# Kernel tuning notes

Measured on AMD Instinct MI355X. Metric: run time of the kernel, lower is better.

Reference implementation:

```python
import jax, jax.numpy as jnp
import numpy as np

HIDDEN = 64
HALF = 32
VOCAB = 64
B, L = 256, 2048


def _l2norm(x):
    # matches torch F.normalize(dim=-1, eps=1e-12)
    return x / jnp.maximum(jnp.linalg.norm(x, axis=-1, keepdims=True), 1e-12)


def setup_inputs() -> dict:
    key = jax.random.key(0)
    ks = jax.random.split(key, 16)
    s = 0.02
    return {
        "seq": jax.random.randint(ks[0], (B, L), 0, VOCAB),
        "embed": jax.random.normal(ks[1], (VOCAB, HIDDEN), jnp.float32) * s,
        "W1": jax.random.normal(ks[2], (2 * HIDDEN, HIDDEN), jnp.float32) * s,
        "b1": jnp.zeros((2 * HIDDEN,), jnp.float32),
        "W2": jax.random.normal(ks[3], (HIDDEN, 2 * HIDDEN), jnp.float32) * s,
        "b2": jnp.zeros((HIDDEN,), jnp.float32),
        "ln_g": jnp.ones((HIDDEN,), jnp.float32),
        "ln_b": jnp.zeros((HIDDEN,), jnp.float32),
        "Ws": jax.random.normal(ks[4], (HALF, HIDDEN), jnp.float32) * s,
        "bs": jnp.zeros((HALF,), jnp.float32),
        "We": jax.random.normal(ks[5], (HALF, HIDDEN), jnp.float32) * s,
        "be": jnp.zeros((HALF,), jnp.float32),
        "Wrp": jax.random.normal(ks[6], (HIDDEN, 2 * HALF), jnp.float32) * s,
        "brp": jnp.zeros((HIDDEN,), jnp.float32),
        "Wo": jax.random.normal(ks[7], (VOCAB, HIDDEN), jnp.float32) * s,
        "bo": jnp.zeros((VOCAB,), jnp.float32),
    }


def reference(seq, embed, W1, b1, W2, b2, ln_g, ln_b, Ws, bs, We, be, Wrp, brp, Wo, bo):
    # Encoder: embed -> LayerNorm(h + FF(h))
    h0 = embed[seq]                                     # [B,L,H]
    ff = jnp.maximum(h0 @ W1.T + b1, 0.0) @ W2.T + b2
    x = h0 + ff
    mu = x.mean(-1, keepdims=True)
    var = x.var(-1, keepdims=True)
    h = (x - mu) / jnp.sqrt(var + 1e-5) * ln_g + ln_b   # [B,L,H]

    Bn, Ln, _ = h.shape
    half = Ws.shape[0]
    hs_all = h @ Ws.T + bs                              # [B,L,half]
    he_all = h @ We.T + be

    # sequential delta-rule memory writes over t = 0 .. L-2
    hs_seq = jnp.swapaxes(hs_all[:, :-1], 0, 1)         # [L-1,B,half]
    he_seq = jnp.swapaxes(he_all[:, :-1], 0, 1)
    scales = (jnp.arange(1, Ln) / Ln).astype(h.dtype)   # (t+1)/L
    M0 = jnp.zeros((Bn, half, half), h.dtype)

    def step(carry, inp):
        M_s, M_e = carry
        hs, he, sc = inp
        ks_ = _l2norm(hs)
        ke_ = _l2norm(he)
        vps = jnp.einsum('bij,bj->bi', M_s, ks_)
        vpe = jnp.einsum('bij,bj->bi', M_e, ke_)
        M_s = M_s + (hs - vps)[:, :, None] * ks_[:, None, :]
        M_e = M_e + sc * (he - vpe)[:, :, None] * ke_[:, None, :]
        return (M_s, M_e), None

    (M_s, M_e), _ = jax.lax.scan(step, (M0, M0), (hs_seq, he_seq, scales))

    # read with last-position query
    qs = _l2norm(hs_all[:, -1])
    qe = _l2norm(he_all[:, -1])
    rs = jnp.einsum('bij,bj->bi', M_s, qs)
    re = jnp.einsum('bij,bj->bi', M_e, qe)
    r = jnp.concatenate([rs, re], axis=-1)              # [B, 2*half]
    return (r @ Wrp.T + brp) @ Wo.T + bo                # [B, vocab]
```

## Files before the change

kernel.cpp:

```cpp
#include <hip/hip_runtime.h>

#define HIDDEN 64
#define HALFD  32
#define VOCAB  64
#define BATCH  256
#define SEQLEN 2048

#define RLF(v, sl) __int_as_float(__builtin_amdgcn_readlane(__float_as_int(v), (sl)))
#define RLI(v, sl) __builtin_amdgcn_readlane((v), (sl))
#define GIX(j,m) (((j)==0?0:(j)==1?7:(j)==2?13:(j)==3?18:(j)==4?22:(j)==5?25:27) + (m) - (j) - 1)
#define OM(m) (((m)*((m)+1))>>1)

__global__ __launch_bounds__(64) void vocab_kernel(
    const float* __restrict__ embed, const float* __restrict__ W1, const float* __restrict__ b1,
    const float* __restrict__ W2, const float* __restrict__ b2,
    const float* __restrict__ ln_g, const float* __restrict__ ln_b,
    const float* __restrict__ Ws, const float* __restrict__ bs,
    const float* __restrict__ We, const float* __restrict__ be,
    float* __restrict__ ws)
{
    const int v = blockIdx.x;
    const int tid = threadIdx.x;

    __shared__ float e_s[64];
    __shared__ float a1_s[128];
    __shared__ float h_s[64];

    e_s[tid] = embed[v * 64 + tid];
    __syncthreads();

    float acc0 = b1[tid], acc1 = b1[tid + 64];
    #pragma unroll 8
    for (int m = 0; m < 64; ++m) {
        float ev = e_s[m];
        acc0 = fmaf(ev, W1[tid * 64 + m], acc0);
        acc1 = fmaf(ev, W1[(tid + 64) * 64 + m], acc1);
    }
    a1_s[tid]      = fmaxf(acc0, 0.0f);
    a1_s[tid + 64] = fmaxf(acc1, 0.0f);
    __syncthreads();

    float ff = b2[tid];
    #pragma unroll 8
    for (int m = 0; m < 128; ++m) ff = fmaf(a1_s[m], W2[tid * 128 + m], ff);
    float x = e_s[tid] + ff;

    float s = x, s2 = x * x;
    #pragma unroll
    for (int off = 32; off >= 1; off >>= 1) {
        s  += __shfl_xor(s,  off, 64);
        s2 += __shfl_xor(s2, off, 64);
    }
    float mu  = s * (1.0f / 64.0f);
    float var = s2 * (1.0f / 64.0f) - mu * mu;
    float hval = (x - mu) * rsqrtf(var + 1e-5f) * ln_g[tid] + ln_b[tid];
    h_s[tid] = hval;
    __syncthreads();

    const int j = tid & 31;
    const bool is_s = tid < 32;
    const float* W = is_s ? Ws : We;
    float acc = is_s ? bs[j] : be[j];
    #pragma unroll 8
    for (int m = 0; m < 64; ++m) acc = fmaf(h_s[m], W[j * 64 + m], acc);

    float n2 = acc * acc;
    #pragma unroll
    for (int off = 16; off >= 1; off >>= 1) n2 += __shfl_xor(n2, off, 64);
    float norm = sqrtf(n2);
    float kn = acc / fmaxf(norm, 1e-12f);

    const int base = v * 32 + j;
    if (is_s) { ws[base]        = kn; ws[4096 + base] = acc; }
    else      { ws[2048 + base] = kn; ws[6144 + base] = acc; }
}

__global__ __launch_bounds__(256) void gram_kernel(float* __restrict__ ws)
{
    const int w = blockIdx.x;
    const int tid = threadIdx.x;
    __shared__ float k_s[2048];
    const float* kb = ws + w * 2048;
    for (int i = tid; i < 2048; i += 256) k_s[i] = kb[i];
    __syncthreads();
    const int a  = tid >> 2;
    const int b0 = (tid & 3) << 4;
    float* Gw = ws + 8192 + w * 4096 + a * 64;
    for (int bb = 0; bb < 16; ++bb) {
        const int bcol = b0 + bb;
        float acc = 0.f;
        #pragma unroll
        for (int m = 0; m < 32; ++m) acc = fmaf(k_s[a * 32 + m], k_s[bcol * 32 + m], acc);
        Gw[bcol] = acc;
    }
}

static __device__ __forceinline__ void build_wpack(
    const int* tj, float fb, float invL, bool is_e, bool is_last, float* Wp,
    const float* __restrict__ Gg)
{
    float f[8];
    #pragma unroll
    for (int j = 0; j < 8; ++j) f[j] = is_e ? (fb + (float)j * invL) : 1.0f;
    if (is_last) f[7] = 0.0f;

    float g[28];
    #pragma unroll
    for (int j = 0; j < 7; ++j)
        #pragma unroll
        for (int m = j + 1; m < 8; ++m) g[GIX(j, m)] = Gg[tj[j] * 64 + tj[m]];

    #pragma unroll
    for (int m = 0; m < 8; ++m) {
        float col[8];
        col[m] = f[m];
        #pragma unroll
        for (int j = 6; j >= 0; --j) {
            if (j < m) {
                float acc = 0.0f;
                #pragma unroll
                for (int p = 1; p < 8; ++p)
                    if (p > j && p <= m) acc = fmaf(g[GIX(j, p)], col[p], acc);
                col[j] = -f[j] * acc;
            }
        }
        #pragma unroll
        for (int j = 0; j < 8; ++j)
            if (j <= m) Wp[OM(m) + j] = col[j];
    }
}

struct Chunk {
    int   tokv;
    int   tk[8];
    float grow[8];
    float W[36];
};

__global__ __launch_bounds__(128) void scan_kernel(
    const int* __restrict__ seq, const float* __restrict__ ws,
    const float* __restrict__ Wrp, const float* __restrict__ brp,
    const float* __restrict__ Wo, const float* __restrict__ bo,
    float* __restrict__ out)
{
    const int b    = blockIdx.x;
    const int tid  = threadIdx.x;
    const int w    = tid >> 6;
    const int lane = tid & 63;
    const int l7   = lane & 7;
    const bool is_e = (w == 1);

    __shared__ __align__(16) float4 Wt4[9][2][256];
    __shared__ __align__(16) int    toklds[SEQLEN];
    __shared__ float wacc_s[2][64];
    __shared__ float r_s[64];
    __shared__ float t1_s[64];

    const float* Gg = ws + 8192 + w * 4096;
    const int*   sq = seq + b * SEQLEN;

    {
        const int4* sq4 = (const int4*)sq;
        int4* tl = (int4*)toklds;
        #pragma unroll
        for (int i = 0; i < 4; ++i) tl[tid + i * 128] = sq4[tid + i * 128];
    }
    __syncthreads();

    {
        const float invL = 1.0f / (float)SEQLEN;
        #pragma unroll
        for (int qq = 0; qq < 4; ++qq) {
            const int c = lane + (qq << 6);
            int tj[8];
            #pragma unroll
            for (int j = 0; j < 8; ++j) tj[j] = toklds[c * 8 + j];
            float Wp[36];
            build_wpack(tj, (float)(8 * c + 1) * invL, invL, is_e, c == 255, Wp, Gg);
            #pragma unroll
            for (int i = 0; i < 9; ++i)
                Wt4[i][w][c] = make_float4(Wp[4*i], Wp[4*i+1], Wp[4*i+2], Wp[4*i+3]);
        }
    }
    __syncthreads();

    Chunk A, B;
    float u, waccv = 0.0f;

    A.tokv = sq[2040 + l7];
    #pragma unroll
    for (int j = 0; j < 8; ++j) A.tk[j] = RLI(A.tokv, j);
    #pragma unroll
    for (int j = 0; j < 8; ++j) A.grow[j] = Gg[A.tk[j] * 64 + lane];
    #pragma unroll
    for (int i = 0; i < 9; ++i) {
        float4 v = Wt4[i][w][255];
        A.W[4*i] = v.x; A.W[4*i+1] = v.y; A.W[4*i+2] = v.z; A.W[4*i+3] = v.w;
    }
    B.tokv = sq[2032 + l7];
    u = Gg[A.tk[7] * 64 + lane];
    float braw = __shfl(u, A.tokv, 64);

    auto body = [&](Chunk& cur, Chunk& nxt, int c) {
        float t0 = RLF(braw, 0), t1 = RLF(braw, 1), t2 = RLF(braw, 2), t3 = RLF(braw, 3);
        float t4 = RLF(braw, 4), t5 = RLF(braw, 5), t6 = RLF(braw, 6), t7 = RLF(braw, 7);

        const int cm1 = (c > 0) ? c - 1 : 0;
        const int cm2 = (c > 1) ? c - 2 : 0;
        #pragma unroll
        for (int j = 0; j < 8; ++j) nxt.tk[j] = RLI(nxt.tokv, j);
        #pragma unroll
        for (int j = 0; j < 8; ++j) nxt.grow[j] = Gg[nxt.tk[j] * 64 + lane];
        #pragma unroll
        for (int i = 0; i < 9; ++i) {
            float4 v = Wt4[i][w][cm1];
            nxt.W[4*i] = v.x; nxt.W[4*i+1] = v.y; nxt.W[4*i+2] = v.z; nxt.W[4*i+3] = v.w;
        }
        int tokv2 = sq[cm2 * 8 + l7];

        const float* W = cur.W;
        float s7 = W[35] * t7;
        float s6 = fmaf(W[27], t6, W[34] * t7);
        float s5 = fmaf(W[20], t5, W[26] * t6) + W[33] * t7;
        float s4 = fmaf(W[14], t4, W[19] * t5) + fmaf(W[25], t6, W[32] * t7);
        float s3 = fmaf(W[9],  t3, W[13] * t4) + fmaf(W[18], t5, fmaf(W[24], t6, W[31] * t7));
        float s2 = fmaf(W[5],  t2, W[8]  * t3) + fmaf(W[12], t4, W[17] * t5) + fmaf(W[23], t6, W[30] * t7);
        float s1 = fmaf(W[2],  t1, W[4]  * t2) + fmaf(W[7],  t3, W[11] * t4) + fmaf(W[16], t5, fmaf(W[22], t6, W[29] * t7));
        float s0 = fmaf(W[0],  t0, W[1]  * t1) + fmaf(W[3],  t2, W[6]  * t3) + fmaf(W[10], t4, W[15] * t5) + fmaf(W[21], t6, W[28] * t7);

        float dA = fmaf(cur.grow[0], s0, fmaf(cur.grow[1], s1, fmaf(cur.grow[2], s2, cur.grow[3] * s3)));
        float dB = fmaf(cur.grow[4], s4, fmaf(cur.grow[5], s5, fmaf(cur.grow[6], s6, cur.grow[7] * s7)));
        u -= (dA + dB);

        braw = __shfl(u, nxt.tokv, 64);

        waccv += (lane == cur.tk[0]) ? s0 : 0.0f;
        waccv += (lane == cur.tk[1]) ? s1 : 0.0f;
        waccv += (lane == cur.tk[2]) ? s2 : 0.0f;
        waccv += (lane == cur.tk[3]) ? s3 : 0.0f;
        waccv += (lane == cur.tk[4]) ? s4 : 0.0f;
        waccv += (lane == cur.tk[5]) ? s5 : 0.0f;
        waccv += (lane == cur.tk[6]) ? s6 : 0.0f;
        waccv += (lane == cur.tk[7]) ? s7 : 0.0f;

        cur.tokv = tokv2;
    };

    for (int c = 255; c >= 1; c -= 2) {
        body(A, B, c);
        body(B, A, c - 1);
    }

    wacc_s[w][lane] = waccv;
    __syncthreads();

    if (tid < 64) {
        const int w2  = tid >> 5;
        const int rho = tid & 31;
        const float* vv = ws + 4096 + w2 * 2048;
        const float* wa = &wacc_s[w2][0];
        float acc = 0.0f;
        #pragma unroll 8
        for (int tok = 0; tok < 64; ++tok) acc = fmaf(wa[tok], vv[tok * 32 + rho], acc);
        r_s[tid] = acc;
    }
    __syncthreads();

    if (tid < 64) {
        float acc = brp[tid];
        #pragma unroll 8
        for (int m = 0; m < 64; ++m) acc = fmaf(Wrp[tid * 64 + m], r_s[m], acc);
        t1_s[tid] = acc;
    }
    __syncthreads();
    if (tid < 64) {
        float acc = bo[tid];
        #pragma unroll 8
        for (int m = 0; m < 64; ++m) acc = fmaf(Wo[tid * 64 + m], t1_s[m], acc);
        out[b * 64 + tid] = acc;
    }
}

extern "C" void kernel_launch(void* const* d_in, const int* in_sizes, int n_in,
                              void* d_out, int out_size, void* d_ws, size_t ws_size,
                              hipStream_t stream)
{
    const int*   seq   = (const int*)  d_in[0];
    const float* embed = (const float*)d_in[1];
    const float* W1    = (const float*)d_in[2];
    const float* b1    = (const float*)d_in[3];
    const float* W2    = (const float*)d_in[4];
    const float* b2    = (const float*)d_in[5];
    const float* ln_g  = (const float*)d_in[6];
    const float* ln_b  = (const float*)d_in[7];
    const float* Ws    = (const float*)d_in[8];
    const float* bs    = (const float*)d_in[9];
    const float* We    = (const float*)d_in[10];
    const float* be    = (const float*)d_in[11];
    const float* Wrp   = (const float*)d_in[12];
    const float* brp   = (const float*)d_in[13];
    const float* Wo    = (const float*)d_in[14];
    const float* bo    = (const float*)d_in[15];
    float* ws  = (float*)d_ws;
    float* out = (float*)d_out;

    hipLaunchKernelGGL(vocab_kernel, dim3(VOCAB), dim3(64), 0, stream,
                       embed, W1, b1, W2, b2, ln_g, ln_b, Ws, bs, We, be, ws);
    hipLaunchKernelGGL(gram_kernel, dim3(2), dim3(256), 0, stream, ws);
    hipLaunchKernelGGL(scan_kernel, dim3(BATCH), dim3(128), 0, stream,
                       seq, ws, Wrp, brp, Wo, bo, out);
}
```

Before: 200.8 us.

## Process 16-step chunks in the backward scan with a cross-block coupling matrix

The sequential backward sweep now handles 16 tokens per iteration instead of 8, halving the number of serial shuffle/readlane round trips. Each chunk is split into two 8-step triangular blocks plus a precomputed 8x8 coupling matrix of Gram entries, all stored in LDS during setup. This shortens the serial dependency chain but increases per-iteration LDS reads (34 float4 vs 9), register pressure, and the serial FMA depth within each step.

```diff
diff --git a/kernel.cpp b/kernel.cpp
--- a/kernel.cpp
+++ b/kernel.cpp
@@ -5,6 +5,7 @@
 #define VOCAB  64
 #define BATCH  256
 #define SEQLEN 2048
+#define NCH    128
 
 #define RLF(v, sl) __int_as_float(__builtin_amdgcn_readlane(__float_as_int(v), (sl)))
 #define RLI(v, sl) __builtin_amdgcn_readlane((v), (sl))
@@ -130,11 +131,23 @@
     }
 }
 
-struct Chunk {
+static __device__ __forceinline__ void apply_w8(
+    const float* __restrict__ W, const float* __restrict__ t, float* __restrict__ s)
+{
+    s[7] = W[35] * t[7];
+    s[6] = fmaf(W[27], t[6], W[34] * t[7]);
+    s[5] = fmaf(W[20], t[5], W[26] * t[6]) + W[33] * t[7];
+    s[4] = fmaf(W[14], t[4], W[19] * t[5]) + fmaf(W[25], t[6], W[32] * t[7]);
+    s[3] = fmaf(W[9],  t[3], W[13] * t[4]) + fmaf(W[18], t[5], fmaf(W[24], t[6], W[31] * t[7]));
+    s[2] = fmaf(W[5],  t[2], W[8]  * t[3]) + fmaf(W[12], t[4], W[17] * t[5]) + fmaf(W[23], t[6], W[30] * t[7]);
+    s[1] = fmaf(W[2],  t[1], W[4]  * t[2]) + fmaf(W[7],  t[3], W[11] * t[4]) + fmaf(W[16], t[5], fmaf(W[22], t[6], W[29] * t[7]));
+    s[0] = fmaf(W[0],  t[0], W[1]  * t[1]) + fmaf(W[3],  t[2], W[6]  * t[3]) + fmaf(W[10], t[4], W[15] * t[5]) + fmaf(W[21], t[6], W[28] * t[7]);
+}
+
+struct Chunk16 {
     int   tokv;
-    int   tk[8];
-    float grow[8];
-    float W[36];
+    int   tk[16];
+    float grow[16];
 };
 
 __global__ __launch_bounds__(128) void scan_kernel(
@@ -147,10 +160,10 @@
     const int tid  = threadIdx.x;
     const int w    = tid >> 6;
     const int lane = tid & 63;
-    const int l7   = lane & 7;
+    const int l15  = lane & 15;
     const bool is_e = (w == 1);
 
-    __shared__ __align__(16) float4 Wt4[9][2][256];
+    __shared__ __align__(16) float4 Wt4[34][2][NCH];
     __shared__ __align__(16) int    toklds[SEQLEN];
     __shared__ float wacc_s[2][64];
     __shared__ float r_s[64];
@@ -170,83 +183,103 @@
     {
         const float invL = 1.0f / (float)SEQLEN;
         #pragma unroll
-        for (int qq = 0; qq < 4; ++qq) {
+        for (int qq = 0; qq < 2; ++qq) {
             const int c = lane + (qq << 6);
-            int tj[8];
+            int tj[16];
             #pragma unroll
-            for (int j = 0; j < 8; ++j) tj[j] = toklds[c * 8 + j];
+            for (int j = 0; j < 16; ++j) tj[j] = toklds[c * 16 + j];
+
             float Wp[36];
-            build_wpack(tj, (float)(8 * c + 1) * invL, invL, is_e, c == 255, Wp, Gg);
+            build_wpack(tj, (float)(16 * c + 1) * invL, invL, is_e, false, Wp, Gg);
             #pragma unroll
             for (int i = 0; i < 9; ++i)
                 Wt4[i][w][c] = make_float4(Wp[4*i], Wp[4*i+1], Wp[4*i+2], Wp[4*i+3]);
-        }
-    }
-    __syncthreads();
-
-    Chunk A, B;
+            build_wpack(tj + 8, (float)(16 * c + 9) * invL, invL, is_e, c == NCH - 1, Wp, Gg);
+            #pragma unroll
+            for (int i = 0; i < 9; ++i)
+                Wt4[9 + i][w][c] = make_float4(Wp[4*i], Wp[4*i+1], Wp[4*i+2], Wp[4*i+3]);
+            #pragma unroll
+            for (int i = 0; i < 16; ++i) {
+                const int j = i >> 1, m0 = (i & 1) << 2;
+                Wt4[18 + i][w][c] = make_float4(
+                    Gg[tj[j] * 64 + tj[8 + m0]],     Gg[tj[j] * 64 + tj[8 + m0 + 1]],
+                    Gg[tj[j] * 64 + tj[8 + m0 + 2]], Gg[tj[j] * 64 + tj[8 + m0 + 3]]);
+            }
+        }
+    }
+    __syncthreads();
+
+    Chunk16 A, B;
     float u, waccv = 0.0f;
 
-    A.tokv = sq[2040 + l7];
-    #pragma unroll
-    for (int j = 0; j < 8; ++j) A.tk[j] = RLI(A.tokv, j);
-    #pragma unroll
-    for (int j = 0; j < 8; ++j) A.grow[j] = Gg[A.tk[j] * 64 + lane];
-    #pragma unroll
-    for (int i = 0; i < 9; ++i) {
-        float4 v = Wt4[i][w][255];
-        A.W[4*i] = v.x; A.W[4*i+1] = v.y; A.W[4*i+2] = v.z; A.W[4*i+3] = v.w;
-    }
-    B.tokv = sq[2032 + l7];
-    u = Gg[A.tk[7] * 64 + lane];
+    A.tokv = sq[(NCH - 1) * 16 + l15];
+    #pragma unroll
+    for (int j = 0; j < 16; ++j) A.tk[j] = RLI(A.tokv, j);
+    #pragma unroll
+    for (int j = 0; j < 16; ++j) A.grow[j] = Gg[A.tk[j] * 64 + lane];
+    B.tokv = sq[(NCH - 2) * 16 + l15];
+    u = Gg[A.tk[15] * 64 + lane];
     float braw = __shfl(u, A.tokv, 64);
 
-    auto body = [&](Chunk& cur, Chunk& nxt, int c) {
-        float t0 = RLF(braw, 0), t1 = RLF(braw, 1), t2 = RLF(braw, 2), t3 = RLF(braw, 3);
-        float t4 = RLF(braw, 4), t5 = RLF(braw, 5), t6 = RLF(braw, 6), t7 = RLF(braw, 7);
-
-        const int cm1 = (c > 0) ? c - 1 : 0;
+    auto body = [&](Chunk16& cur, Chunk16& nxt, int c) {
+        float t[16];
+        #pragma unroll
+        for (int j = 0; j < 16; ++j) t[j] = RLF(braw, j);
+
         const int cm2 = (c > 1) ? c - 2 : 0;
         #pragma unroll
-        for (int j = 0; j < 8; ++j) nxt.tk[j] = RLI(nxt.tokv, j);
-        #pragma unroll
-        for (int j = 0; j < 8; ++j) nxt.grow[j] = Gg[nxt.tk[j] * 64 + lane];
+        for (int j = 0; j < 16; ++j) nxt.tk[j] = RLI(nxt.tokv, j);
+        #pragma unroll
+        for (int j = 0; j < 16; ++j) nxt.grow[j] = Gg[nxt.tk[j] * 64 + lane];
+        int tokv2 = sq[cm2 * 16 + l15];
+
+        float Wa[36], Wb[36], U[64];
         #pragma unroll
         for (int i = 0; i < 9; ++i) {
-            float4 v = Wt4[i][w][cm1];
-            nxt.W[4*i] = v.x; nxt.W[4*i+1] = v.y; nxt.W[4*i+2] = v.z; nxt.W[4*i+3] = v.w;
-        }
-        int tokv2 = sq[cm2 * 8 + l7];
-
-        const float* W = cur.W;
-        float s7 = W[35] * t7;
-        float s6 = fmaf(W[27], t6, W[34] * t7);
-        float s5 = fmaf(W[20], t5, W[26] * t6) + W[33] * t7;
-        float s4 = fmaf(W[14], t4, W[19] * t5) + fmaf(W[25], t6, W[32] * t7);
-        float s3 = fmaf(W[9],  t3, W[13] * t4) + fmaf(W[18], t5, fmaf(W[24], t6, W[31] * t7));
-        float s2 = fmaf(W[5],  t2, W[8]  * t3) + fmaf(W[12], t4, W[17] * t5) + fmaf(W[23], t6, W[30] * t7);
-        float s1 = fmaf(W[2],  t1, W[4]  * t2) + fmaf(W[7],  t3, W[11] * t4) + fmaf(W[16], t5, fmaf(W[22], t6, W[29] * t7));
-        float s0 = fmaf(W[0],  t0, W[1]  * t1) + fmaf(W[3],  t2, W[6]  * t3) + fmaf(W[10], t4, W[15] * t5) + fmaf(W[21], t6, W[28] * t7);
-
-        float dA = fmaf(cur.grow[0], s0, fmaf(cur.grow[1], s1, fmaf(cur.grow[2], s2, cur.grow[3] * s3)));
-        float dB = fmaf(cur.grow[4], s4, fmaf(cur.grow[5], s5, fmaf(cur.grow[6], s6, cur.grow[7] * s7)));
-        u -= (dA + dB);
+            float4 v = Wt4[i][w][c];
+            Wa[4*i] = v.x; Wa[4*i+1] = v.y; Wa[4*i+2] = v.z; Wa[4*i+3] = v.w;
+        }
+        #pragma unroll
+        for (int i = 0; i < 9; ++i) {
+            float4 v = Wt4[9 + i][w][c];
+            Wb[4*i] = v.x; Wb[4*i+1] = v.y; Wb[4*i+2] = v.z; Wb[4*i+3] = v.w;
+        }
+        #pragma unroll
+        for (int i = 0; i < 16; ++i) {
+            float4 v = Wt4[18 + i][w][c];
+            U[4*i] = v.x; U[4*i+1] = v.y; U[4*i+2] = v.z; U[4*i+3] = v.w;
+        }
+
+        float sb[8], sa[8], ta[8];
+        apply_w8(Wb, t + 8, sb);
+        #pragma unroll
+        for (int j = 0; j < 8; ++j) {
+            const float* Uj = U + j * 8;
+            float y0 = fmaf(Uj[0], sb[0], Uj[1] * sb[1]);
+            float y1 = fmaf(Uj[2], sb[2], Uj[3] * sb[3]);
+            float y2 = fmaf(Uj[4], sb[4], Uj[5] * sb[5]);
+            float y3 = fmaf(Uj[6], sb[6], Uj[7] * sb[7]);
+            ta[j] = t[j] - ((y0 + y1) + (y2 + y3));
+        }
+        apply_w8(Wa, ta, sa);
+
+        float d0 = fmaf(cur.grow[0],  sa[0], fmaf(cur.grow[1],  sa[1], fmaf(cur.grow[2],  sa[2], cur.grow[3]  * sa[3])));
+        float d1 = fmaf(cur.grow[4],  sa[4], fmaf(cur.grow[5],  sa[5], fmaf(cur.grow[6],  sa[6], cur.grow[7]  * sa[7])));
+        float d2 = fmaf(cur.grow[8],  sb[0], fmaf(cur.grow[9],  sb[1], fmaf(cur.grow[10], sb[2], cur.grow[11] * sb[3])));
+        float d3 = fmaf(cur.grow[12], sb[4], fmaf(cur.grow[13], sb[5], fmaf(cur.grow[14], sb[6], cur.grow[15] * sb[7])));
+        u -= ((d0 + d1) + (d2 + d3));
 
         braw = __shfl(u, nxt.tokv, 64);
 
-        waccv += (lane == cur.tk[0]) ? s0 : 0.0f;
-        waccv += (lane == cur.tk[1]) ? s1 : 0.0f;
-        waccv += (lane == cur.tk[2]) ? s2 : 0.0f;
-        waccv += (lane == cur.tk[3]) ? s3 : 0.0f;
-        waccv += (lane == cur.tk[4]) ? s4 : 0.0f;
-        waccv += (lane == cur.tk[5]) ? s5 : 0.0f;
-        waccv += (lane == cur.tk[6]) ? s6 : 0.0f;
-        waccv += (lane == cur.tk[7]) ? s7 : 0.0f;
+        #pragma unroll
+        for (int j = 0; j < 8; ++j) waccv += (lane == cur.tk[j])     ? sa[j] : 0.0f;
+        #pragma unroll
+        for (int j = 0; j < 8; ++j) waccv += (lane == cur.tk[8 + j]) ? sb[j] : 0.0f;
 
         cur.tokv = tokv2;
     };
 
-    for (int c = 255; c >= 1; c -= 2) {
+    for (int c = NCH - 1; c >= 1; c -= 2) {
         body(A, B, c);
         body(B, A, c - 1);
     }
```

After: 231.2 us. 15.2% more time.
